# Kernel optimization log

Measured on AMD Instinct MI355X. Metric: run time of the kernel, lower is better.

## Reference

```python
import jax, jax.numpy as jnp
import numpy as np
import math

B, S, D = 2, 2048, 2048
H = 16
DK = D // H


def build_rotary(dim, seq_len):
    inv_freq = 1.0 / (10000.0 ** (np.arange(0, dim, 2, dtype=np.float32) / dim))
    t = np.arange(seq_len, dtype=np.float32)
    freqs = np.einsum('i,j->ij', t, inv_freq)
    emb = np.concatenate([freqs, freqs], axis=-1)  # [S, dim]
    return jnp.asarray(np.cos(emb))[None, None], jnp.asarray(np.sin(emb))[None, None]


def rotate_half(x):
    x1, x2 = jnp.split(x, 2, axis=-1)
    return jnp.concatenate([-x2, x1], axis=-1)


def setup_inputs() -> dict:
    key = jax.random.key(0)
    ks = jax.random.split(key, 12)
    s = 1.0 / math.sqrt(D)
    inp = {
        'query': jax.random.normal(ks[0], (B, S, D), jnp.float32),
        'key': jax.random.normal(ks[1], (B, S, D), jnp.float32),
        'value': jax.random.normal(ks[2], (B, S, D), jnp.float32),
        'mask': jnp.tril(jnp.ones((S, S), bool))[None, None],  # causal [1,1,S,S]
        'wq': jax.random.uniform(ks[3], (D, D), jnp.float32, -s, s),
        'bq': jax.random.uniform(ks[4], (D,), jnp.float32, -s, s),
        'wk': jax.random.uniform(ks[5], (D, D), jnp.float32, -s, s),
        'bk': jax.random.uniform(ks[6], (D,), jnp.float32, -s, s),
        'wv': jax.random.uniform(ks[7], (D, D), jnp.float32, -s, s),
        'bv': jax.random.uniform(ks[8], (D,), jnp.float32, -s, s),
        'wo': jax.random.uniform(ks[9], (D, D), jnp.float32, -s, s),
        'bo': jax.random.uniform(ks[10], (D,), jnp.float32, -s, s),
    }
    return inp


def reference(query, key, value, mask, wq, bq, wk, bk, wv, bv, wo, bo):
    Bc, Sc, _ = query.shape
    # QKV projections -> [B, H, S, DK]
    def proj(x, w, b):
        return (x @ w.T + b).reshape(Bc, Sc, H, DK).transpose(0, 2, 1, 3)
    q = proj(query, wq, bq)
    k = proj(key, wk, bk)
    v = proj(value, wv, bv)
    # inline RoPE
    cos, sin = build_rotary(DK, Sc)
    cos = cos.astype(query.dtype)
    sin = sin.astype(query.dtype)
    q = q * cos + rotate_half(q) * sin
    k = k * cos + rotate_half(k) * sin
    # attention (dropout in eval / identity)
    scores = jnp.einsum('bhqd,bhkd->bhqk', q, k) / math.sqrt(DK)
    scores = jnp.where(mask, scores.astype(jnp.float32), -1e9)
    p = jax.nn.softmax(scores, axis=-1)
    x = jnp.einsum('bhqk,bhkd->bhqd', p, v)
    x = x.transpose(0, 2, 1, 3).reshape(Bc, Sc, H * DK)
    return x @ wo.T + bo
```

## Files before the change

### kernel.cpp

```cpp
#include <hip/hip_runtime.h>
#include <hip/hip_bf16.h>

#define Bc 2
#define Sc 2048
#define Dc 2048
#define Hc 16
#define DKc 128
#define Mc (Bc * Sc)
#define Kc Dc
#define Nc Dc
#define NX ((size_t)Bc * Sc * Dc)
#define NW ((size_t)Dc * Dc)
#define NTK (Kc / 32)

#define SM_C 0.1275174366f

typedef unsigned short u16;
using bf16x8  = __bf16 __attribute__((ext_vector_type(8)));
using ushort8 = unsigned short __attribute__((ext_vector_type(8)));
using ushort4v = unsigned short __attribute__((ext_vector_type(4)));
using floatx4 = float __attribute__((ext_vector_type(4)));
using float4v = float __attribute__((ext_vector_type(4)));

__device__ __forceinline__ u16 f2bf(float f) {
  union { float f; unsigned u; } x; x.f = f;
  unsigned r = x.u + 0x7fffu + ((x.u >> 16) & 1u);
  return (u16)(r >> 16);
}
__device__ __forceinline__ float bf2f(u16 u) {
  union { unsigned u; float f; } x; x.u = ((unsigned)u) << 16;
  return x.f;
}
__device__ __forceinline__ bf16x8 load8(const u16* p) {
  return __builtin_bit_cast(bf16x8, *(const ushort8*)p);
}
__device__ __forceinline__ floatx4 mfma16(bf16x8 a, bf16x8 b, floatx4 c) {
  return __builtin_amdgcn_mfma_f32_16x16x32_bf16(a, b, c, 0, 0, 0);
}
__device__ __forceinline__ void async16(const void* g, void* l) {
  __builtin_amdgcn_global_load_lds(
      (__attribute__((address_space(1))) void*)(g),
      (__attribute__((address_space(3))) void*)(l), 16, 0, 0);
}

__global__ __launch_bounds__(256) void cast_all(
    const float* __restrict__ q, const float* __restrict__ k,
    const float* __restrict__ v, const float* __restrict__ wq,
    const float* __restrict__ wk, const float* __restrict__ wv,
    const float* __restrict__ wo, u16* __restrict__ dst) {
  size_t i4 = (size_t)blockIdx.x * 256 + threadIdx.x;
  size_t e = i4 * 4;
  const float* src; size_t off;
  if (e < 3 * NX) {
    size_t w = e / NX;
    src = (w == 0) ? q : (w == 1) ? k : v;
    off = e - w * NX;
  } else {
    size_t e2 = e - 3 * NX;
    size_t w = e2 / NW;
    src = (w == 0) ? wq : (w == 1) ? wk : (w == 2) ? wv : wo;
    off = e2 - w * NW;
  }
  float4v val = *(const float4v*)(src + off);
  ushort4v o;
  o.x = f2bf(val.x); o.y = f2bf(val.y); o.z = f2bf(val.z); o.w = f2bf(val.w);
  *(ushort4v*)(dst + e) = o;
}

__device__ __forceinline__ void gemm_body(
    const u16* __restrict__ A, const u16* __restrict__ W,
    const float* __restrict__ bias, u16* __restrict__ out_bf,
    float* __restrict__ out_f, int epi, int m0, int n0,
    u16* __restrict__ lds ) {
  const int tid = threadIdx.x;
  const int wid = tid >> 6, lane = tid & 63;
  const int l15 = lane & 15, quad = lane >> 4;
  const int wm = wid >> 1, wn = wid & 1;

  const int sr = tid >> 2;
  const int sc = ((tid & 3) ^ ((tid >> 3) & 3)) * 8;
  const u16* gA = A + (size_t)(m0 + sr) * Kc + sc;
  const u16* gB = W + (size_t)(n0 + sr) * Kc + sc;
  const size_t half = (size_t)64 * Kc;

  const int slot8 = (quad ^ ((l15 >> 1) & 3)) * 8;
  const int arow0 = (wm * 64 + l15) * 32 + slot8;
  const int brow0 = 4096 + (wn * 64 + l15) * 32 + slot8;

  floatx4 acc[4][4] = {};

  u16* b0 = lds;
  u16* b1 = lds + 8192;
  u16* b2 = lds + 16384;

  async16(gA,             b0 + tid * 8);
  async16(gA + half,      b0 + 2048 + tid * 8);
  async16(gB,             b0 + 4096 + tid * 8);
  async16(gB + half,      b0 + 6144 + tid * 8);
  async16(gA + 32,        b1 + tid * 8);
  async16(gA + 32 + half, b1 + 2048 + tid * 8);
  async16(gB + 32,        b1 + 4096 + tid * 8);
  async16(gB + 32 + half, b1 + 6144 + tid * 8);
  asm volatile("s_waitcnt vmcnt(4)" ::: "memory");
  __builtin_amdgcn_s_barrier();

  const u16* gAt = gA + 64;
  const u16* gBt = gB + 64;

  for (int t = 0; t < NTK; ++t) {
    if (t < NTK - 2) {
      async16(gAt,        b2 + tid * 8);
      async16(gAt + half, b2 + 2048 + tid * 8);
      async16(gBt,        b2 + 4096 + tid * 8);
      async16(gBt + half, b2 + 6144 + tid * 8);
    }

    bf16x8 af[4], bfr[4];
#pragma unroll
    for (int m = 0; m < 4; ++m) af[m] = load8(b0 + arow0 + m * 512);
#pragma unroll
    for (int n = 0; n < 4; ++n) bfr[n] = load8(b0 + brow0 + n * 512);

    __builtin_amdgcn_s_setprio(1);
#pragma unroll
    for (int m = 0; m < 4; ++m)
#pragma unroll
      for (int n = 0; n < 4; ++n)
        acc[m][n] = mfma16(af[m], bfr[n], acc[m][n]);
    __builtin_amdgcn_s_setprio(0);

    if (t < NTK - 2)       asm volatile("s_waitcnt vmcnt(4)" ::: "memory");
    else if (t == NTK - 2) asm volatile("s_waitcnt vmcnt(0)" ::: "memory");
    __builtin_amdgcn_s_barrier();

    u16* tmp = b0; b0 = b1; b1 = b2; b2 = tmp;
    gAt += 32; gBt += 32;
  }

#pragma unroll
  for (int n = 0; n < 4; ++n) {
    int col = n0 + wn * 64 + n * 16 + l15;
    float bv = bias[col];
#pragma unroll
    for (int m = 0; m < 4; ++m) {
      int rowb = m0 + wm * 64 + m * 16 + quad * 4;
#pragma unroll
      for (int r = 0; r < 4; ++r) {
        float v = acc[m][n][r] + bv;
        int row = rowb + r;
        if (epi == 2) {
          out_f[(size_t)row * Nc + col] = v;
        } else {
          int b = row >> 11, s = row & 2047;
          int h = col >> 7, dk = col & 127;
          size_t addr = (epi == 0)
              ? ((size_t)(b * Hc + h) * Sc + s) * DKc + dk
              : ((size_t)(b * Hc + h) * DKc + dk) * Sc + s;
          out_bf[addr] = f2bf(v);
        }
      }
    }
  }
}

__global__ __launch_bounds__(256, 3) void gemm_qkv(
    const u16* __restrict__ xq, const u16* __restrict__ xk,
    const u16* __restrict__ xv, const u16* __restrict__ wcat,
    const float* __restrict__ bq, const float* __restrict__ bk,
    const float* __restrict__ bv, u16* __restrict__ qhw,
    u16* __restrict__ khw, u16* __restrict__ vtw) {
  __shared__ u16 lds[3 * 8192];
  const int proj = blockIdx.z;
  const int n0 = blockIdx.x * 128;
  const int m0 = blockIdx.y * 128;
  const u16* A = (proj == 0) ? xq : (proj == 1) ? xk : xv;
  const u16* W = wcat + (size_t)proj * 2048 * Kc;
  const float* bias = (proj == 0) ? bq : (proj == 1) ? bk : bv;
  u16* outp = (proj == 0) ? qhw : (proj == 1) ? khw : vtw;
  gemm_body(A, W, bias, outp, nullptr, (proj == 2) ? 1 : 0, m0, n0, lds);
}

__global__ __launch_bounds__(256, 3) void gemm_out(
    const u16* __restrict__ A, const u16* __restrict__ W,
    const float* __restrict__ bias, float* __restrict__ out_f) {
  __shared__ u16 lds[3 * 8192];
  gemm_body(A, W, bias, nullptr, out_f, 2, blockIdx.y * 128,
            blockIdx.x * 128, lds);
}

__global__ __launch_bounds__(256) void rope_kernel(u16* __restrict__ q,
                                                   u16* __restrict__ k) {
  int i = blockIdx.x * 256 + threadIdx.x;
  int d = i & 63;
  int s = (i >> 6) & (Sc - 1);
  int bh = i >> 17;
  size_t base = ((size_t)bh * Sc + s) * DKc;
  float inv_freq = exp2f((float)d * (-13.287712379549449f / 64.0f));
  float ang = (float)s * inv_freq;
  float sn, cs;
  sincosf(ang, &sn, &cs);
  float q1 = bf2f(q[base + d]), q2 = bf2f(q[base + d + 64]);
  q[base + d]      = f2bf((q1 * cs - q2 * sn) * SM_C);
  q[base + d + 64] = f2bf((q2 * cs + q1 * sn) * SM_C);
  float k1 = bf2f(k[base + d]), k2 = bf2f(k[base + d + 64]);
  k[base + d]      = f2bf(k1 * cs - k2 * sn);
  k[base + d + 64] = f2bf(k2 * cs + k1 * sn);
}

__global__ __launch_bounds__(256) void attn_kernel(
    const u16* __restrict__ qh, const u16* __restrict__ kh,
    const u16* __restrict__ vt, u16* __restrict__ ao) {
  __shared__ u16 Ksl[128 * 128];
  __shared__ u16 Vsl[144 * 128];
  const int tid = threadIdx.x;
  const int wid = tid >> 6, lane = tid & 63;
  const int l15 = lane & 15, quad = lane >> 4;
  const int qt = (blockIdx.z == 0) ? 15 - (int)blockIdx.x : (int)blockIdx.x;
  const int h = blockIdx.y, bb = blockIdx.z;
  const int bh = bb * Hc + h;
  const int q0 = qt * 128;
  const u16* qbase = qh + (size_t)bh * Sc * DKc;
  const u16* kbase = kh + (size_t)bh * Sc * DKc;
  const u16* vbase = vt + (size_t)bh * DKc * Sc;

  const int srow = tid >> 4;
  const int scol = (tid & 15) * 8;
  const int sdst = ((tid & 15) ^ srow) * 8;

  {
    int r = 128 + srow;
    u16 val = (r == 128) ? (u16)0x3F80 : (u16)0;
#pragma unroll
    for (int j = 0; j < 8; j++) Vsl[r * 128 + scol + j] = val;
  }

  bf16x8 qf[2][4];
#pragma unroll
  for (int mt = 0; mt < 2; mt++)
#pragma unroll
    for (int kq = 0; kq < 4; kq++)
      qf[mt][kq] = load8(qbase + (size_t)(q0 + wid * 32 + mt * 16 + l15) * DKc +
                         kq * 32 + quad * 8);

  floatx4 accO[2][9] = {};

  ushort8 kr[8], vr[8];
#pragma unroll
  for (int c = 0; c < 8; c++) {
    int rr = c * 16 + srow;
    kr[c] = *(const ushort8*)(kbase + (size_t)rr * DKc + scol);
    vr[c] = *(const ushort8*)(vbase + (size_t)rr * Sc + scol);
  }

  for (int kt = 0; kt <= qt; kt++) {
    __syncthreads();
#pragma unroll
    for (int c = 0; c < 8; c++) {
      int rr = c * 16 + srow;
      *(ushort8*)&Ksl[rr * 128 + sdst] = kr[c];
      *(ushort8*)&Vsl[rr * 128 + sdst] = vr[c];
    }
    __syncthreads();

    floatx4 sacc[2][8] = {};
#pragma unroll
    for (int kk = 0; kk < 4; kk++) {
      const int sb = ((kk * 4 + quad) ^ l15) * 8;
#pragma unroll
      for (int nt = 0; nt < 8; nt++) {
        bf16x8 kf = load8(&Ksl[(nt * 16 + l15) * 128 + sb]);
        sacc[0][nt] = mfma16(qf[0][kk], kf, sacc[0][nt]);
        sacc[1][nt] = mfma16(qf[1][kk], kf, sacc[1][nt]);
      }
    }

    if (kt == qt) {
#pragma unroll
      for (int nt = 0; nt < 8; nt++) {
        int kcol = nt * 16 + l15;
#pragma unroll
        for (int mt = 0; mt < 2; mt++) {
          int qrow = wid * 32 + mt * 16 + quad * 4;
#pragma unroll
          for (int r = 0; r < 4; r++)
            if (kcol > qrow + r) sacc[mt][nt][r] = -1e30f;
        }
      }
    }

#pragma unroll
    for (int mt = 0; mt < 2; mt++)
#pragma unroll
      for (int nt = 0; nt < 8; nt++)
#pragma unroll
        for (int r = 0; r < 4; r++)
          sacc[mt][nt][r] = exp2f(sacc[mt][nt][r]);

    __syncthreads();

    u16* Pw = &Ksl[wid * 4096];
#pragma unroll
    for (int mt = 0; mt < 2; mt++)
#pragma unroll
      for (int nt = 0; nt < 8; nt++)
#pragma unroll
        for (int r = 0; r < 4; r++) {
          int row = mt * 16 + quad * 4 + r;
          int col = nt * 16 + l15;
          int sb = (col >> 3) ^ (row & 15);
          Pw[row * 128 + sb * 8 + (col & 7)] = f2bf(sacc[mt][nt][r]);
        }

    if (kt < qt) {
      const u16* kb = kbase + (size_t)(kt + 1) * 128 * DKc;
#pragma unroll
      for (int c = 0; c < 8; c++) {
        int rr = c * 16 + srow;
        kr[c] = *(const ushort8*)(kb + (size_t)rr * DKc + scol);
        vr[c] = *(const ushort8*)(vbase + (size_t)rr * Sc + (kt + 1) * 128 + scol);
      }
    }

#pragma unroll
    for (int kk = 0; kk < 4; kk++) {
      const int sb = ((kk * 4 + quad) ^ l15) * 8;
      bf16x8 pf0 = load8(&Pw[(0 * 16 + l15) * 128 + sb]);
      bf16x8 pf1 = load8(&Pw[(1 * 16 + l15) * 128 + sb]);
#pragma unroll
      for (int nt = 0; nt < 9; nt++) {
        bf16x8 vf = load8(&Vsl[(nt * 16 + l15) * 128 + sb]);
        accO[0][nt] = mfma16(pf0, vf, accO[0][nt]);
        accO[1][nt] = mfma16(pf1, vf, accO[1][nt]);
      }
    }
  }

#pragma unroll
  for (int mt = 0; mt < 2; mt++)
#pragma unroll
    for (int r = 0; r < 4; r++) {
      float lsum = __shfl(accO[mt][8][r], lane & 48);
      float inv = 1.0f / lsum;
      int gq = q0 + wid * 32 + mt * 16 + quad * 4 + r;
      size_t rowbase = ((size_t)bb * Sc + gq) * Dc + h * DKc;
#pragma unroll
      for (int nt = 0; nt < 8; nt++)
        ao[rowbase + nt * 16 + l15] = f2bf(accO[mt][nt][r] * inv);
    }
}

extern "C" void kernel_launch(void* const* d_in, const int* in_sizes, int n_in,
                              void* d_out, int out_size, void* d_ws,
                              size_t ws_size, hipStream_t stream) {
  const float* q  = (const float*)d_in[0];
  const float* k  = (const float*)d_in[1];
  const float* v  = (const float*)d_in[2];
  const float* wq = (const float*)d_in[4];
  const float* bq = (const float*)d_in[5];
  const float* wk = (const float*)d_in[6];
  const float* bk = (const float*)d_in[7];
  const float* wv = (const float*)d_in[8];
  const float* bv = (const float*)d_in[9];
  const float* wo = (const float*)d_in[10];
  const float* bo = (const float*)d_in[11];
  float* out = (float*)d_out;

  u16* ws = (u16*)d_ws;
  u16* xq  = ws;
  u16* xk  = ws + NX;
  u16* xv  = ws + 2 * NX;
  u16* wcat = ws + 3 * NX;
  u16* wob = ws + 3 * NX + 3 * NW;
  u16* qhw = ws + 3 * NX + 4 * NW;
  u16* khw = ws + 4 * NX + 4 * NW;
  u16* vtw = ws + 5 * NX + 4 * NW;
  u16* aow = ws + 6 * NX + 4 * NW;

  {
    size_t tot4 = (3 * NX + 4 * NW) / 4;
    cast_all<<<dim3((unsigned)(tot4 / 256)), 256, 0, stream>>>(
        q, k, v, wq, wk, wv, wo, ws);
  }
  gemm_qkv<<<dim3(Nc / 128, Mc / 128, 3), 256, 0, stream>>>(
      xq, xk, xv, wcat, bq, bk, bv, qhw, khw, vtw);
  rope_kernel<<<dim3(Bc * Hc * Sc * 64 / 256), 256, 0, stream>>>(qhw, khw);
  attn_kernel<<<dim3(Sc / 128, Hc, Bc), 256, 0, stream>>>(qhw, khw, vtw, aow);
  gemm_out<<<dim3(Nc / 128, Mc / 128), 256, 0, stream>>>(aow, wob, bo, out);
}
```

Measured before the change: 508.5 us.

## Fuse RoPE and softmax scaling into QKV GEMM epilogue, drop rope kernel

Each wave's N-columns are remapped so that it holds both column d and d+64 of a head in registers. This lets the QKV GEMM epilogue apply the rotary embedding (and the softmax scale for Q) directly before storing bf16. The separate rope kernel is removed, along with its read-modify-write pass over Q and K. In exchange, every output element in the epilogue now pays for a sincosf call, and the B-fragment LDS access pattern changes.

Measured after the change: 504.2 us. No clear change (-0.9%).

```diff
diff --git a/kernel.cpp b/kernel.cpp
--- a/kernel.cpp
+++ b/kernel.cpp
@@ -14,6 +14,7 @@
 #define NTK (Kc / 32)
 
 #define SM_C 0.1275174366f
+#define L2_10000 13.287712379549449f
 
 typedef unsigned short u16;
 using bf16x8  = __bf16 __attribute__((ext_vector_type(8)));
@@ -70,7 +71,7 @@
 __device__ __forceinline__ void gemm_body(
     const u16* __restrict__ A, const u16* __restrict__ W,
     const float* __restrict__ bias, u16* __restrict__ out_bf,
-    float* __restrict__ out_f, int epi, int m0, int n0,
+    float* __restrict__ out_f, int mode, int m0, int n0,
     u16* __restrict__ lds ) {
   const int tid = threadIdx.x;
   const int wid = tid >> 6, lane = tid & 63;
@@ -85,7 +86,7 @@
 
   const int slot8 = (quad ^ ((l15 >> 1) & 3)) * 8;
   const int arow0 = (wm * 64 + l15) * 32 + slot8;
-  const int brow0 = 4096 + (wn * 64 + l15) * 32 + slot8;
+  const int brow0 = 4096 + (wn * 32 + l15) * 32 + slot8;
 
   floatx4 acc[4][4] = {};
 
@@ -118,8 +119,10 @@
     bf16x8 af[4], bfr[4];
 #pragma unroll
     for (int m = 0; m < 4; ++m) af[m] = load8(b0 + arow0 + m * 512);
-#pragma unroll
-    for (int n = 0; n < 4; ++n) bfr[n] = load8(b0 + brow0 + n * 512);
+    bfr[0] = load8(b0 + brow0);
+    bfr[1] = load8(b0 + brow0 + 512);
+    bfr[2] = load8(b0 + brow0 + 2048);
+    bfr[3] = load8(b0 + brow0 + 2560);
 
     __builtin_amdgcn_s_setprio(1);
 #pragma unroll
@@ -138,25 +141,42 @@
   }
 
 #pragma unroll
-  for (int n = 0; n < 4; ++n) {
-    int col = n0 + wn * 64 + n * 16 + l15;
-    float bv = bias[col];
+  for (int n2 = 0; n2 < 2; ++n2) {
+    int col_lo = n0 + wn * 32 + n2 * 16 + l15;
+    int col_hi = col_lo + 64;
+    float blo = bias[col_lo], bhi = bias[col_hi];
+    float invf = 0.0f;
+    if (mode <= 1) {
+      int d = col_lo & 127;
+      invf = exp2f((float)d * (-L2_10000 / 64.0f));
+    }
 #pragma unroll
     for (int m = 0; m < 4; ++m) {
       int rowb = m0 + wm * 64 + m * 16 + quad * 4;
 #pragma unroll
       for (int r = 0; r < 4; ++r) {
-        float v = acc[m][n][r] + bv;
         int row = rowb + r;
-        if (epi == 2) {
-          out_f[(size_t)row * Nc + col] = v;
+        float vlo = acc[m][n2][r] + blo;
+        float vhi = acc[m][n2 + 2][r] + bhi;
+        int b = row >> 11, s = row & 2047;
+        if (mode <= 1) {
+          float sn, cs;
+          sincosf((float)s * invf, &sn, &cs);
+          float rlo = vlo * cs - vhi * sn;
+          float rhi = vhi * cs + vlo * sn;
+          if (mode == 0) { rlo *= SM_C; rhi *= SM_C; }
+          int h = col_lo >> 7;
+          size_t base = ((size_t)(b * Hc + h) * Sc + s) * DKc;
+          out_bf[base + (col_lo & 127)] = f2bf(rlo);
+          out_bf[base + (col_hi & 127)] = f2bf(rhi);
+        } else if (mode == 2) {
+          int h = col_lo >> 7;
+          size_t basev = (size_t)(b * Hc + h) * DKc;
+          out_bf[(basev + (col_lo & 127)) * Sc + s] = f2bf(vlo);
+          out_bf[(basev + (col_hi & 127)) * Sc + s] = f2bf(vhi);
         } else {
-          int b = row >> 11, s = row & 2047;
-          int h = col >> 7, dk = col & 127;
-          size_t addr = (epi == 0)
-              ? ((size_t)(b * Hc + h) * Sc + s) * DKc + dk
-              : ((size_t)(b * Hc + h) * DKc + dk) * Sc + s;
-          out_bf[addr] = f2bf(v);
+          out_f[(size_t)row * Nc + col_lo] = vlo;
+          out_f[(size_t)row * Nc + col_hi] = vhi;
         }
       }
     }
@@ -177,34 +197,15 @@
   const u16* W = wcat + (size_t)proj * 2048 * Kc;
   const float* bias = (proj == 0) ? bq : (proj == 1) ? bk : bv;
   u16* outp = (proj == 0) ? qhw : (proj == 1) ? khw : vtw;
-  gemm_body(A, W, bias, outp, nullptr, (proj == 2) ? 1 : 0, m0, n0, lds);
+  gemm_body(A, W, bias, outp, nullptr, proj, m0, n0, lds);
 }
 
 __global__ __launch_bounds__(256, 3) void gemm_out(
     const u16* __restrict__ A, const u16* __restrict__ W,
     const float* __restrict__ bias, float* __restrict__ out_f) {
   __shared__ u16 lds[3 * 8192];
-  gemm_body(A, W, bias, nullptr, out_f, 2, blockIdx.y * 128,
+  gemm_body(A, W, bias, nullptr, out_f, 3, blockIdx.y * 128,
             blockIdx.x * 128, lds);
-}
-
-__global__ __launch_bounds__(256) void rope_kernel(u16* __restrict__ q,
-                                                   u16* __restrict__ k) {
-  int i = blockIdx.x * 256 + threadIdx.x;
-  int d = i & 63;
-  int s = (i >> 6) & (Sc - 1);
-  int bh = i >> 17;
-  size_t base = ((size_t)bh * Sc + s) * DKc;
-  float inv_freq = exp2f((float)d * (-13.287712379549449f / 64.0f));
-  float ang = (float)s * inv_freq;
-  float sn, cs;
-  sincosf(ang, &sn, &cs);
-  float q1 = bf2f(q[base + d]), q2 = bf2f(q[base + d + 64]);
-  q[base + d]      = f2bf((q1 * cs - q2 * sn) * SM_C);
-  q[base + d + 64] = f2bf((q2 * cs + q1 * sn) * SM_C);
-  float k1 = bf2f(k[base + d]), k2 = bf2f(k[base + d + 64]);
-  k[base + d]      = f2bf(k1 * cs - k2 * sn);
-  k[base + d + 64] = f2bf(k2 * cs + k1 * sn);
 }
 
 __global__ __launch_bounds__(256) void attn_kernel(
@@ -383,7 +384,6 @@
   }
   gemm_qkv<<<dim3(Nc / 128, Mc / 128, 3), 256, 0, stream>>>(
       xq, xk, xv, wcat, bq, bk, bv, qhw, khw, vtw);
-  rope_kernel<<<dim3(Bc * Hc * Sc * 64 / 256), 256, 0, stream>>>(qhw, khw);
   attn_kernel<<<dim3(Sc / 128, Hc, Bc), 256, 0, stream>>>(qhw, khw, vtw, aow);
   gemm_out<<<dim3(Nc / 128, Mc / 128), 256, 0, stream>>>(aow, wob, bo, out);
 }
```
